# Kernel tuning notes

Measured on AMD Instinct MI355X. Metric: run time of the kernel, lower is better.

The kernel has to match this reference:

```python
import jax, jax.numpy as jnp
import numpy as np

N_QUBITS = 6
N_LAYERS = 3
BATCH = 4194304


def setup_inputs() -> dict:
    key = jax.random.key(0)
    k1, k2, k3 = jax.random.split(key, 3)
    x = jax.random.uniform(k1, (BATCH, N_QUBITS), dtype=jnp.float32)
    rotation_params = jax.random.normal(k2, (N_LAYERS, N_QUBITS, 3), dtype=jnp.float32) * 0.1
    entanglement_params = jax.random.normal(k3, (N_LAYERS, N_QUBITS - 1), dtype=jnp.float32) * 0.1
    return {"x": x, "rotation_params": rotation_params, "entanglement_params": entanglement_params}


def reference(x, rotation_params, entanglement_params):
    n_layers = rotation_params.shape[0]
    # Initial angle encoding: state[i] = (cos(pi*x_i/2), sin(pi*x_i/2))
    half = x * (jnp.pi * 0.5)  # [B, Q]
    state_real = jnp.cos(half)
    state_imag = jnp.sin(half)
    for layer in range(n_layers):
        # RX-style rotation (only the first rotation param is used per qubit)
        rx = rotation_params[layer, :, 0]  # [Q]
        c = jnp.cos(rx * 0.5)
        s = jnp.sin(rx * 0.5)
        new_real = c * state_real + s * state_imag
        new_imag = c * state_imag - s * state_real
        state_real, state_imag = new_real, new_imag
        # Entanglement: sequential in-place loop in torch reduces to this closed
        # form because entangled[i+1] written at step i is overwritten at step
        # i+1 (all reads are from the pre-entanglement state_real).
        strength = jax.nn.sigmoid(entanglement_params[layer])  # [Q-1]
        avg = (state_real[:, :-1] + state_real[:, 1:]) * 0.5    # [B, Q-1]
        left = (1.0 - strength) * state_real[:, :-1] + strength * avg  # cols 0..Q-2
        last = (1.0 - strength[-1]) * state_real[:, -1] + strength[-1] * avg[:, -1]
        state_real = jnp.concatenate([left, last[:, None]], axis=1)
    return jnp.sqrt(state_real ** 2 + state_imag ** 2)
```

## Files before the change

### kernel.cpp

```cpp
#include <hip/hip_runtime.h>
#include <math.h>

#define N_QUBITS 6
#define N_LAYERS 3

__global__ __launch_bounds__(256) void qc_kernel(
    const float* __restrict__ x,
    const float* __restrict__ rot,
    const float* __restrict__ ent,
    float* __restrict__ out,
    int n_pairs)
{
    __shared__ float sc[N_LAYERS][N_QUBITS];
    __shared__ float ss[N_LAYERS][N_QUBITS];
    __shared__ float sst[N_LAYERS][N_QUBITS - 1];

    const int t = threadIdx.x;
    if (t < N_LAYERS * N_QUBITS) {
        const int l = t / N_QUBITS, q = t % N_QUBITS;
        const float rx = rot[(l * N_QUBITS + q) * 3 + 0];
        float s_, c_;
        sincosf(rx * 0.5f, &s_, &c_);
        sc[l][q] = c_;
        ss[l][q] = s_;
    } else if (t < N_LAYERS * N_QUBITS + N_LAYERS * (N_QUBITS - 1)) {
        const int u = t - N_LAYERS * N_QUBITS;
        const int l = u / (N_QUBITS - 1), j = u % (N_QUBITS - 1);
        const float e = ent[l * (N_QUBITS - 1) + j];
        sst[l][j] = 1.0f / (1.0f + expf(-e));
    }
    __syncthreads();

    const int idx = blockIdx.x * blockDim.x + threadIdx.x;
    if (idx >= n_pairs) return;

    const float4* __restrict__ xin = (const float4*)(x + (size_t)idx * 12);
    float4 va = xin[0];
    float4 vb = xin[1];
    float4 vc = xin[2];
    float v[12] = {va.x, va.y, va.z, va.w,
                   vb.x, vb.y, vb.z, vb.w,
                   vc.x, vc.y, vc.z, vc.w};
    float o[12];

#pragma unroll
    for (int r0 = 0; r0 < 2; ++r0) {
        float re[N_QUBITS], im[N_QUBITS];
#pragma unroll
        for (int q = 0; q < N_QUBITS; ++q) {
            const float rev = v[r0 * 6 + q] * 0.25f;
            im[q] = __builtin_amdgcn_sinf(rev);
            re[q] = __builtin_amdgcn_cosf(rev);
        }
#pragma unroll
        for (int l = 0; l < N_LAYERS; ++l) {
#pragma unroll
            for (int q = 0; q < N_QUBITS; ++q) {
                const float c_ = sc[l][q], s_ = ss[l][q];
                const float nr = c_ * re[q] + s_ * im[q];
                const float ni = c_ * im[q] - s_ * re[q];
                re[q] = nr;
                im[q] = ni;
            }
            float avg[N_QUBITS - 1];
#pragma unroll
            for (int j = 0; j < N_QUBITS - 1; ++j)
                avg[j] = (re[j] + re[j + 1]) * 0.5f;
            float nr_[N_QUBITS];
#pragma unroll
            for (int j = 0; j < N_QUBITS - 1; ++j) {
                const float st = sst[l][j];
                nr_[j] = (1.0f - st) * re[j] + st * avg[j];
            }
            {
                const float st = sst[l][N_QUBITS - 2];
                nr_[N_QUBITS - 1] =
                    (1.0f - st) * re[N_QUBITS - 1] + st * avg[N_QUBITS - 2];
            }
#pragma unroll
            for (int q = 0; q < N_QUBITS; ++q) re[q] = nr_[q];
        }
#pragma unroll
        for (int q = 0; q < N_QUBITS; ++q)
            o[r0 * 6 + q] = sqrtf(re[q] * re[q] + im[q] * im[q]);
    }

    float4* __restrict__ dst = (float4*)(out + (size_t)idx * 12);
    dst[0] = make_float4(o[0], o[1], o[2], o[3]);
    dst[1] = make_float4(o[4], o[5], o[6], o[7]);
    dst[2] = make_float4(o[8], o[9], o[10], o[11]);
}

extern "C" void kernel_launch(void* const* d_in, const int* in_sizes, int n_in,
                              void* d_out, int out_size, void* d_ws, size_t ws_size,
                              hipStream_t stream) {
    const float* x   = (const float*)d_in[0];
    const float* rot = (const float*)d_in[1];
    const float* ent = (const float*)d_in[2];
    float* out = (float*)d_out;

    const int n_rows  = in_sizes[0] / N_QUBITS;
    const int n_pairs = n_rows / 2;
    const int block = 256;
    const int grid = (n_pairs + block - 1) / block;

    qc_kernel<<<grid, block, 0, stream>>>(x, rot, ent, out, n_pairs);
}
```

Baseline: 182.0 us.

## Precompute gate constants in a prep kernel and process four rows per thread

Gate cosines, sines and sigmoid strengths are moved into a tiny prep kernel that writes a 52-float table into the workspace. The main kernel then loads that table into scalar registers through readfirstlane instead of building it in shared memory behind a __syncthreads in every block. Each thread now handles four rows instead of two, with six float4 loads and stores issued as two batches, and uses the hardware sqrt intrinsic. The aim is to remove per-block setup and sync and to raise bytes in flight per thread. In exchange it adds a second launch, raises register pressure, and silently drops any row count that is not a multiple of four.

```diff
diff --git a/kernel.cpp b/kernel.cpp
--- a/kernel.cpp
+++ b/kernel.cpp
@@ -4,51 +4,62 @@
 #define N_QUBITS 6
 #define N_LAYERS 3
 
-__global__ __launch_bounds__(256) void qc_kernel(
+__global__ void prep_kernel(const float* __restrict__ rot,
+                            const float* __restrict__ ent,
+                            float* __restrict__ tbl) {
+    const int t = threadIdx.x;
+    if (t < 18) {
+        const int l = t / 6, q = t % 6;
+        float s_, c_;
+        sincosf(rot[(l * 6 + q) * 3] * 0.5f, &s_, &c_);
+        tbl[t] = c_;
+        tbl[18 + t] = s_;
+    } else if (t < 33) {
+        const int u = t - 18;
+        tbl[36 + u] = 1.0f / (1.0f + expf(-ent[u]));
+    } else if (t == 33) {
+        tbl[51] = 0.0f;
+    }
+}
+
+__global__ __launch_bounds__(256) void qc_main(
     const float* __restrict__ x,
-    const float* __restrict__ rot,
-    const float* __restrict__ ent,
+    const float* __restrict__ tbl,
     float* __restrict__ out,
-    int n_pairs)
+    int n_threads)
 {
-    __shared__ float sc[N_LAYERS][N_QUBITS];
-    __shared__ float ss[N_LAYERS][N_QUBITS];
-    __shared__ float sst[N_LAYERS][N_QUBITS - 1];
+    const int idx = blockIdx.x * blockDim.x + threadIdx.x;
+    if (idx >= n_threads) return;
 
-    const int t = threadIdx.x;
-    if (t < N_LAYERS * N_QUBITS) {
-        const int l = t / N_QUBITS, q = t % N_QUBITS;
-        const float rx = rot[(l * N_QUBITS + q) * 3 + 0];
-        float s_, c_;
-        sincosf(rx * 0.5f, &s_, &c_);
-        sc[l][q] = c_;
-        ss[l][q] = s_;
-    } else if (t < N_LAYERS * N_QUBITS + N_LAYERS * (N_QUBITS - 1)) {
-        const int u = t - N_LAYERS * N_QUBITS;
-        const int l = u / (N_QUBITS - 1), j = u % (N_QUBITS - 1);
-        const float e = ent[l * (N_QUBITS - 1) + j];
-        sst[l][j] = 1.0f / (1.0f + expf(-e));
+    float cst[52];
+    const float4* __restrict__ t4 = (const float4*)tbl;
+#pragma unroll
+    for (int i = 0; i < 13; ++i) {
+        const float4 w = t4[i];
+        cst[4 * i + 0] = __int_as_float(__builtin_amdgcn_readfirstlane(__float_as_int(w.x)));
+        cst[4 * i + 1] = __int_as_float(__builtin_amdgcn_readfirstlane(__float_as_int(w.y)));
+        cst[4 * i + 2] = __int_as_float(__builtin_amdgcn_readfirstlane(__float_as_int(w.z)));
+        cst[4 * i + 3] = __int_as_float(__builtin_amdgcn_readfirstlane(__float_as_int(w.w)));
     }
-    __syncthreads();
+#define CC(l, q) cst[(l) * 6 + (q)]
+#define SS(l, q) cst[18 + (l) * 6 + (q)]
+#define ST(l, j) cst[36 + (l) * 5 + (j)]
 
-    const int idx = blockIdx.x * blockDim.x + threadIdx.x;
-    if (idx >= n_pairs) return;
+    const float4* __restrict__ xin = (const float4*)x + (size_t)idx * 6;
+    float4 in[6];
+#pragma unroll
+    for (int i = 0; i < 6; ++i) in[i] = xin[i];
+    const float* vp = (const float*)in;
 
-    const float4* __restrict__ xin = (const float4*)(x + (size_t)idx * 12);
-    float4 va = xin[0];
-    float4 vb = xin[1];
-    float4 vc = xin[2];
-    float v[12] = {va.x, va.y, va.z, va.w,
-                   vb.x, vb.y, vb.z, vb.w,
-                   vc.x, vc.y, vc.z, vc.w};
-    float o[12];
+    float4* __restrict__ dst = (float4*)out + (size_t)idx * 6;
+    float o12[12];
 
 #pragma unroll
-    for (int r0 = 0; r0 < 2; ++r0) {
+    for (int r = 0; r < 4; ++r) {
         float re[N_QUBITS], im[N_QUBITS];
 #pragma unroll
         for (int q = 0; q < N_QUBITS; ++q) {
-            const float rev = v[r0 * 6 + q] * 0.25f;
+            const float rev = vp[r * 6 + q] * 0.25f;
             im[q] = __builtin_amdgcn_sinf(rev);
             re[q] = __builtin_amdgcn_cosf(rev);
         }
@@ -56,7 +67,7 @@
         for (int l = 0; l < N_LAYERS; ++l) {
 #pragma unroll
             for (int q = 0; q < N_QUBITS; ++q) {
-                const float c_ = sc[l][q], s_ = ss[l][q];
+                const float c_ = CC(l, q), s_ = SS(l, q);
                 const float nr = c_ * re[q] + s_ * im[q];
                 const float ni = c_ * im[q] - s_ * re[q];
                 re[q] = nr;
@@ -69,11 +80,11 @@
             float nr_[N_QUBITS];
 #pragma unroll
             for (int j = 0; j < N_QUBITS - 1; ++j) {
-                const float st = sst[l][j];
+                const float st = ST(l, j);
                 nr_[j] = (1.0f - st) * re[j] + st * avg[j];
             }
             {
-                const float st = sst[l][N_QUBITS - 2];
+                const float st = ST(l, N_QUBITS - 2);
                 nr_[N_QUBITS - 1] =
                     (1.0f - st) * re[N_QUBITS - 1] + st * avg[N_QUBITS - 2];
             }
@@ -82,13 +93,19 @@
         }
 #pragma unroll
         for (int q = 0; q < N_QUBITS; ++q)
-            o[r0 * 6 + q] = sqrtf(re[q] * re[q] + im[q] * im[q]);
+            o12[(r & 1) * 6 + q] =
+                __builtin_amdgcn_sqrtf(re[q] * re[q] + im[q] * im[q]);
+
+        if (r & 1) {
+            const int base = (r >> 1) * 3;
+            dst[base + 0] = make_float4(o12[0], o12[1], o12[2], o12[3]);
+            dst[base + 1] = make_float4(o12[4], o12[5], o12[6], o12[7]);
+            dst[base + 2] = make_float4(o12[8], o12[9], o12[10], o12[11]);
+        }
     }
-
-    float4* __restrict__ dst = (float4*)(out + (size_t)idx * 12);
-    dst[0] = make_float4(o[0], o[1], o[2], o[3]);
-    dst[1] = make_float4(o[4], o[5], o[6], o[7]);
-    dst[2] = make_float4(o[8], o[9], o[10], o[11]);
+#undef CC
+#undef SS
+#undef ST
 }
 
 extern "C" void kernel_launch(void* const* d_in, const int* in_sizes, int n_in,
@@ -98,11 +115,13 @@
     const float* rot = (const float*)d_in[1];
     const float* ent = (const float*)d_in[2];
     float* out = (float*)d_out;
+    float* tbl = (float*)d_ws;
 
-    const int n_rows  = in_sizes[0] / N_QUBITS;
-    const int n_pairs = n_rows / 2;
+    const int n_rows    = in_sizes[0] / N_QUBITS;
+    const int n_threads = n_rows / 4;
     const int block = 256;
-    const int grid = (n_pairs + block - 1) / block;
+    const int grid = (n_threads + block - 1) / block;
 
-    qc_kernel<<<grid, block, 0, stream>>>(x, rot, ent, out, n_pairs);
+    prep_kernel<<<1, 64, 0, stream>>>(rot, ent, tbl);
+    qc_main<<<grid, block, 0, stream>>>(x, tbl, out, n_threads);
 }
```

New measurement: 205.4 us. 1.13x slower.
